# Kernel optimization log

Measured on AMD Instinct MI355X. Metric: run time of the kernel, lower is better.

Reference implementation:

```python
import jax, jax.numpy as jnp
import numpy as np

EMPHASIS_FACTOR = 1.5

def setup_inputs() -> dict:
    key = jax.random.key(0)
    k1, k2 = jax.random.split(key)
    B, T, F = 32, 4096, 256
    x = jax.random.normal(k1, (B, T, F), dtype=jnp.float32)
    W = jax.random.normal(k2, (F, 1), dtype=jnp.float32) * (1.0 / np.sqrt(F))
    b = jnp.zeros((1,), dtype=jnp.float32)
    return {"x": x, "W": W, "b": b}

def reference(x, W, b):
    # x: [B, T, F], W: [F, 1], b: [1]
    B, T, F = x.shape
    e = jnp.tanh(x @ W + b)                 # [B, T, 1]
    a = jax.nn.softmax(e, axis=1)           # softmax over time
    a_flat = a[..., 0]                      # [B, T]
    k = max(1, int(T * 0.1))
    _, top_idx = jax.lax.top_k(a_flat, k)   # [B, k]
    # scatter True at top-k positions (instead of O(T*k) broadcast compare)
    mask = jnp.zeros((B, T), dtype=bool).at[jnp.arange(B)[:, None], top_idx].set(True)
    a_emph = jnp.where(mask[..., None], a * EMPHASIS_FACTOR, a)  # [B, T, 1]
    return jnp.sum(x * a_emph, axis=1, keepdims=True)            # [B, 1, F]
```

## Files before the change

### kernel.cpp

```cpp
#include <hip/hip_runtime.h>
#include <math.h>

#define BB 32
#define TT 4096
#define FF 256
#define CH 64
#define NC (TT / CH)
#define K_TOP 409
#define EMPH_HALF 0.5f

__device__ __forceinline__ unsigned flip_key(float v) {
    unsigned u = __float_as_uint(v);
    return (u & 0x80000000u) ? ~u : (u | 0x80000000u);
}
__device__ __forceinline__ float unflip_key(unsigned k) {
    unsigned u = (k & 0x80000000u) ? (k & 0x7fffffffu) : ~k;
    return __uint_as_float(u);
}
__device__ __forceinline__ float fast_tanh(float z) {
    z = fminf(fmaxf(z, -15.f), 15.f);
    const float t = __expf(2.f * z);
    return (t - 1.f) * __builtin_amdgcn_rcpf(t + 1.f);
}

__global__ __launch_bounds__(256) void fused_pass1(const float* __restrict__ x,
                                                   const float* __restrict__ W,
                                                   const float* __restrict__ bias,
                                                   float* __restrict__ e,
                                                   float* __restrict__ P,
                                                   float* __restrict__ cm,
                                                   float* __restrict__ cs) {
    const int b = blockIdx.x / NC;
    const int c = blockIdx.x % NC;
    const int tid = threadIdx.x;
    const int wv = tid >> 6, ln = tid & 63;

    const float* xc = x + ((size_t)b * TT + (size_t)c * CH) * FF;
    const float4 wvec = ((const float4*)W)[ln];
    const float  bb   = bias[0];

    float4 acc = make_float4(0.f, 0.f, 0.f, 0.f);
    float  m = -1e30f, ssum = 0.f;

    #pragma unroll
    for (int s0 = 0; s0 < CH; s0 += 16) {
        const int r0 = s0 + wv * 4;
        float4 xr[4];
        #pragma unroll
        for (int i = 0; i < 4; i++)
            xr[i] = ((const float4*)(xc + (size_t)(r0 + i) * FF))[ln];

        float dv[4];
        #pragma unroll
        for (int i = 0; i < 4; i++)
            dv[i] = xr[i].x * wvec.x + xr[i].y * wvec.y +
                    xr[i].z * wvec.z + xr[i].w * wvec.w;
        #pragma unroll
        for (int i = 0; i < 4; i++) {
            float d = dv[i];
            #pragma unroll
            for (int off = 32; off; off >>= 1) d += __shfl_xor(d, off);
            dv[i] = fast_tanh(d + bb);
        }
        if (ln == 0)
            *(float4*)(e + (size_t)b * TT + c * CH + r0) =
                make_float4(dv[0], dv[1], dv[2], dv[3]);

        float lm = m;
        #pragma unroll
        for (int i = 0; i < 4; i++) lm = fmaxf(lm, dv[i]);
        const float alpha = __expf(m - lm);
        acc.x *= alpha; acc.y *= alpha; acc.z *= alpha; acc.w *= alpha;
        ssum *= alpha;
        #pragma unroll
        for (int i = 0; i < 4; i++) {
            const float wgt = __expf(dv[i] - lm);
            ssum += wgt;
            acc.x += wgt * xr[i].x; acc.y += wgt * xr[i].y;
            acc.z += wgt * xr[i].z; acc.w += wgt * xr[i].w;
        }
        m = lm;
    }

    __shared__ float4 part4[4][64];
    __shared__ float sm[4], ss4[4];
    part4[wv][ln] = acc;
    if (ln == 0) { sm[wv] = m; ss4[wv] = ssum; }
    __syncthreads();

    const float m0 = sm[0], m1 = sm[1], m2 = sm[2], m3 = sm[3];
    const float mc = fmaxf(fmaxf(m0, m1), fmaxf(m2, m3));
    const float s0s = __expf(m0 - mc), s1s = __expf(m1 - mc);
    const float s2s = __expf(m2 - mc), s3s = __expf(m3 - mc);
    const float* pf = (const float*)part4;
    const float p = pf[tid] * s0s + pf[256 + tid] * s1s +
                    pf[512 + tid] * s2s + pf[768 + tid] * s3s;
    P[((size_t)b * NC + c) * FF + tid] = p;
    if (tid == 0) {
        cm[b * NC + c] = mc;
        cs[b * NC + c] = ss4[0] * s0s + ss4[1] * s1s + ss4[2] * s2s + ss4[3] * s3s;
    }
}

__global__ __launch_bounds__(256) void select_combine(const float* __restrict__ x,
                                                      const float* __restrict__ e,
                                                      const float* __restrict__ P,
                                                      const float* __restrict__ cm,
                                                      const float* __restrict__ cs,
                                                      float* __restrict__ out) {
    const int b = blockIdx.x;
    const int tid = threadIdx.x;
    const int wv = tid >> 6, ln = tid & 63;

    __shared__ float sgm, sZ;
    __shared__ int   sc4[4];
    __shared__ float sscale[NC];
    __shared__ int   scount;
    __shared__ int   slist[TT];
    __shared__ float sval[TT];

    if (tid < 64) {
        const float mm = cm[b * NC + tid];
        const float ss = cs[b * NC + tid];
        float g = mm;
        #pragma unroll
        for (int off = 32; off; off >>= 1) g = fmaxf(g, __shfl_xor(g, off));
        float zz = ss * __expf(mm - g);
        #pragma unroll
        for (int off = 32; off; off >>= 1) zz += __shfl_xor(zz, off);
        if (tid == 0) { sgm = g; sZ = zz; scount = 0; }
    }

    const float* eb = e + (size_t)b * TT;
    unsigned key[16];
    #pragma unroll
    for (int j = 0; j < 16; j++) key[j] = flip_key(eb[tid + 256 * j]);
    __syncthreads();
    if (tid < 64) sscale[tid] = __expf(cm[b * NC + tid] - sgm);

    unsigned prefix = 0u, mask = 0u;
    int kk = K_TOP;
    for (int bit = 31; bit >= 0; bit--) {
        const unsigned bm = 1u << bit;
        const unsigned m2 = mask | bm;
        const unsigned want = prefix | bm;
        int cnt = 0;
        #pragma unroll
        for (int j = 0; j < 16; j++)
            cnt += (int)__popcll(__ballot((key[j] & m2) == want));
        __syncthreads();
        if (ln == 0) sc4[wv] = cnt;
        __syncthreads();
        const int tot = sc4[0] + sc4[1] + sc4[2] + sc4[3];
        if (tot >= kk) prefix = want; else kk -= tot;
        mask = m2;
    }
    const unsigned Kkey = prefix;

    float acc = 0.f;
    #pragma unroll 4
    for (int c = 0; c < NC; c++)
        acc += P[((size_t)b * NC + c) * FF + tid] * sscale[c];

    #pragma unroll
    for (int j = 0; j < 16; j++) {
        if (key[j] >= Kkey) {
            const int i = atomicAdd(&scount, 1);
            slist[i] = tid + 256 * j;
            sval[i]  = unflip_key(key[j]);
        }
    }
    __syncthreads();
    const int n = scount;
    for (int i = tid; i < n; i += 256)
        sval[i] = EMPH_HALF * __expf(sval[i] - sgm);
    __syncthreads();

    const float* xb = x + (size_t)b * TT * FF;
    for (int i = 0; i < n; i++)
        acc += sval[i] * xb[(size_t)slist[i] * FF + tid];

    out[b * FF + tid] = acc * (1.f / sZ);
}

extern "C" void kernel_launch(void* const* d_in, const int* in_sizes, int n_in,
                              void* d_out, int out_size, void* d_ws, size_t ws_size,
                              hipStream_t stream) {
    const float* x    = (const float*)d_in[0];
    const float* W    = (const float*)d_in[1];
    const float* bias = (const float*)d_in[2];
    float* out = (float*)d_out;

    float* e     = (float*)d_ws;
    float* P     = e + (size_t)BB * TT;
    float* cm    = P + (size_t)BB * NC * FF;
    float* cs    = cm + BB * NC;

    fused_pass1<<<BB * NC, 256, 0, stream>>>(x, W, bias, e, P, cm, cs);
    select_combine<<<BB, 256, 0, stream>>>(x, e, P, cm, cs, out);
}
```

Before: 231.0 us.

## Split select and combine into separate kernels, parallelize combine across time segments

The single per-batch select+combine kernel becomes two kernels. The first computes the radix-select threshold and softmax stats per batch and writes them to workspace. The second runs 16 blocks per batch, each handling a time segment, and accumulates into the output with atomics. The combine's strided gathers of selected rows were serialized over 32 blocks, and spreading them across more blocks raises parallelism. In exchange it adds a kernel launch, float atomics on the output, and summation order that can vary between runs.

```diff
diff --git a/kernel.cpp b/kernel.cpp
--- a/kernel.cpp
+++ b/kernel.cpp
@@ -8,6 +8,9 @@
 #define NC (TT / CH)
 #define K_TOP 409
 #define EMPH_HALF 0.5f
+#define NSEG 16
+#define SEGT (TT / NSEG)
+#define CPS (NC / NSEG)
 
 __device__ __forceinline__ unsigned flip_key(float v) {
     unsigned u = __float_as_uint(v);
@@ -102,22 +105,19 @@
     }
 }
 
-__global__ __launch_bounds__(256) void select_combine(const float* __restrict__ x,
-                                                      const float* __restrict__ e,
-                                                      const float* __restrict__ P,
-                                                      const float* __restrict__ cm,
-                                                      const float* __restrict__ cs,
-                                                      float* __restrict__ out) {
+__global__ __launch_bounds__(256) void select_kernel(const float* __restrict__ e,
+                                                     const float* __restrict__ cm,
+                                                     const float* __restrict__ cs,
+                                                     float* __restrict__ stats,
+                                                     float* __restrict__ out) {
     const int b = blockIdx.x;
     const int tid = threadIdx.x;
     const int wv = tid >> 6, ln = tid & 63;
 
+    out[b * FF + tid] = 0.f;
+
     __shared__ float sgm, sZ;
     __shared__ int   sc4[4];
-    __shared__ float sscale[NC];
-    __shared__ int   scount;
-    __shared__ int   slist[TT];
-    __shared__ float sval[TT];
 
     if (tid < 64) {
         const float mm = cm[b * NC + tid];
@@ -128,15 +128,13 @@
         float zz = ss * __expf(mm - g);
         #pragma unroll
         for (int off = 32; off; off >>= 1) zz += __shfl_xor(zz, off);
-        if (tid == 0) { sgm = g; sZ = zz; scount = 0; }
+        if (tid == 0) { sgm = g; sZ = zz; }
     }
 
     const float* eb = e + (size_t)b * TT;
     unsigned key[16];
     #pragma unroll
     for (int j = 0; j < 16; j++) key[j] = flip_key(eb[tid + 256 * j]);
-    __syncthreads();
-    if (tid < 64) sscale[tid] = __expf(cm[b * NC + tid] - sgm);
 
     unsigned prefix = 0u, mask = 0u;
     int kk = K_TOP;
@@ -155,32 +153,57 @@
         if (tot >= kk) prefix = want; else kk -= tot;
         mask = m2;
     }
-    const unsigned Kkey = prefix;
+
+    if (tid == 0) {
+        stats[3 * b + 0] = sgm;
+        stats[3 * b + 1] = sZ;
+        stats[3 * b + 2] = __uint_as_float(prefix);
+    }
+}
+
+__global__ __launch_bounds__(256) void combine_kernel(const float* __restrict__ x,
+                                                      const float* __restrict__ e,
+                                                      const float* __restrict__ P,
+                                                      const float* __restrict__ cm,
+                                                      const float* __restrict__ stats,
+                                                      float* __restrict__ out) {
+    const int b = blockIdx.x / NSEG;
+    const int s = blockIdx.x % NSEG;
+    const int tid = threadIdx.x;
+
+    const float gmax = stats[3 * b + 0];
+    const float Z    = stats[3 * b + 1];
+    const unsigned Kkey = __float_as_uint(stats[3 * b + 2]);
 
     float acc = 0.f;
-    #pragma unroll 4
-    for (int c = 0; c < NC; c++)
-        acc += P[((size_t)b * NC + c) * FF + tid] * sscale[c];
-
     #pragma unroll
-    for (int j = 0; j < 16; j++) {
-        if (key[j] >= Kkey) {
-            const int i = atomicAdd(&scount, 1);
-            slist[i] = tid + 256 * j;
-            sval[i]  = unflip_key(key[j]);
-        }
-    }
+    for (int c = 0; c < CPS; c++) {
+        const int cc = s * CPS + c;
+        const float sc2 = __expf(cm[b * NC + cc] - gmax);
+        acc += P[((size_t)b * NC + cc) * FF + tid] * sc2;
+    }
+
+    __shared__ int scount;
+    __shared__ int slist[SEGT];
+    __shared__ float sval[SEGT];
+    if (tid == 0) scount = 0;
     __syncthreads();
+
+    const int t = s * SEGT + tid;
+    const float ev = e[(size_t)b * TT + t];
+    if (flip_key(ev) >= Kkey) {
+        const int i = atomicAdd(&scount, 1);
+        slist[i] = t;
+        sval[i] = EMPH_HALF * __expf(ev - gmax);
+    }
+    __syncthreads();
+
     const int n = scount;
-    for (int i = tid; i < n; i += 256)
-        sval[i] = EMPH_HALF * __expf(sval[i] - sgm);
-    __syncthreads();
-
     const float* xb = x + (size_t)b * TT * FF;
     for (int i = 0; i < n; i++)
         acc += sval[i] * xb[(size_t)slist[i] * FF + tid];
 
-    out[b * FF + tid] = acc * (1.f / sZ);
+    atomicAdd(&out[b * FF + tid], acc * (1.f / Z));
 }
 
 extern "C" void kernel_launch(void* const* d_in, const int* in_sizes, int n_in,
@@ -195,7 +218,9 @@
     float* P     = e + (size_t)BB * TT;
     float* cm    = P + (size_t)BB * NC * FF;
     float* cs    = cm + BB * NC;
+    float* stats = cs + BB * NC;
 
     fused_pass1<<<BB * NC, 256, 0, stream>>>(x, W, bias, e, P, cm, cs);
-    select_combine<<<BB, 256, 0, stream>>>(x, e, P, cm, cs, out);
-}
+    select_kernel<<<BB, 256, 0, stream>>>(e, cm, cs, stats, out);
+    combine_kernel<<<BB * NSEG, 256, 0, stream>>>(x, e, P, cm, stats, out);
+}
```

Result: faster. 209.7 us (-9.2%).

## Split select/combine across time segments per batch with atomic output accumulation

Applied to the files above, without the earlier changes.

The second kernel now runs 16 blocks per batch instead of one. Each block redundantly computes the top-k threshold, then gathers only the selected rows in its own time segment and its share of the chunk partials, and adds its result into the output with atomicAdd. The output is zeroed in the first kernel. The radix-select loop drops one barrier per bit by giving each bit its own shared slot. The aim is to spread the serial gather over many more CUs, at the cost of repeating the threshold search and adding float atomics with nondeterministic summation order.

```diff
diff --git a/kernel.cpp b/kernel.cpp
--- a/kernel.cpp
+++ b/kernel.cpp
@@ -8,6 +8,9 @@
 #define NC (TT / CH)
 #define K_TOP 409
 #define EMPH_HALF 0.5f
+#define NSEG 16
+#define SEGT (TT / NSEG)
+#define CPS (NC / NSEG)
 
 __device__ __forceinline__ unsigned flip_key(float v) {
     unsigned u = __float_as_uint(v);
@@ -29,11 +32,14 @@
                                                    float* __restrict__ e,
                                                    float* __restrict__ P,
                                                    float* __restrict__ cm,
-                                                   float* __restrict__ cs) {
+                                                   float* __restrict__ cs,
+                                                   float* __restrict__ out) {
     const int b = blockIdx.x / NC;
     const int c = blockIdx.x % NC;
     const int tid = threadIdx.x;
     const int wv = tid >> 6, ln = tid & 63;
+
+    if (c == 0) out[b * FF + tid] = 0.f;
 
     const float* xc = x + ((size_t)b * TT + (size_t)c * CH) * FF;
     const float4 wvec = ((const float4*)W)[ln];
@@ -102,22 +108,24 @@
     }
 }
 
-__global__ __launch_bounds__(256) void select_combine(const float* __restrict__ x,
+__global__ __launch_bounds__(256) void combine_kernel(const float* __restrict__ x,
                                                       const float* __restrict__ e,
                                                       const float* __restrict__ P,
                                                       const float* __restrict__ cm,
                                                       const float* __restrict__ cs,
                                                       float* __restrict__ out) {
-    const int b = blockIdx.x;
+    const int b = blockIdx.x / NSEG;
+    const int s = blockIdx.x % NSEG;
     const int tid = threadIdx.x;
     const int wv = tid >> 6, ln = tid & 63;
 
     __shared__ float sgm, sZ;
-    __shared__ int   sc4[4];
-    __shared__ float sscale[NC];
+    __shared__ int   sc[32][4];
     __shared__ int   scount;
-    __shared__ int   slist[TT];
-    __shared__ float sval[TT];
+    __shared__ int   slist[SEGT];
+    __shared__ float sval[SEGT];
+
+    if (tid == 0) scount = 0;
 
     if (tid < 64) {
         const float mm = cm[b * NC + tid];
@@ -128,59 +136,58 @@
         float zz = ss * __expf(mm - g);
         #pragma unroll
         for (int off = 32; off; off >>= 1) zz += __shfl_xor(zz, off);
-        if (tid == 0) { sgm = g; sZ = zz; scount = 0; }
+        if (tid == 0) { sgm = g; sZ = zz; }
     }
 
     const float* eb = e + (size_t)b * TT;
     unsigned key[16];
     #pragma unroll
     for (int j = 0; j < 16; j++) key[j] = flip_key(eb[tid + 256 * j]);
+
     __syncthreads();
-    if (tid < 64) sscale[tid] = __expf(cm[b * NC + tid] - sgm);
+    const float gmax = sgm;
+    const float Zinv = 1.f / sZ;
+
+    float acc = 0.f;
+    #pragma unroll
+    for (int c = 0; c < CPS; c++) {
+        const int cc = s * CPS + c;
+        acc += P[((size_t)b * NC + cc) * FF + tid] * __expf(cm[b * NC + cc] - gmax);
+    }
 
     unsigned prefix = 0u, mask = 0u;
     int kk = K_TOP;
-    for (int bit = 31; bit >= 0; bit--) {
-        const unsigned bm = 1u << bit;
+    #pragma unroll 4
+    for (int it = 0; it < 32; it++) {
+        const unsigned bm = 1u << (31 - it);
         const unsigned m2 = mask | bm;
         const unsigned want = prefix | bm;
         int cnt = 0;
         #pragma unroll
         for (int j = 0; j < 16; j++)
             cnt += (int)__popcll(__ballot((key[j] & m2) == want));
+        if (ln == 0) sc[it][wv] = cnt;
         __syncthreads();
-        if (ln == 0) sc4[wv] = cnt;
-        __syncthreads();
-        const int tot = sc4[0] + sc4[1] + sc4[2] + sc4[3];
+        const int tot = sc[it][0] + sc[it][1] + sc[it][2] + sc[it][3];
         if (tot >= kk) prefix = want; else kk -= tot;
         mask = m2;
     }
     const unsigned Kkey = prefix;
 
-    float acc = 0.f;
-    #pragma unroll 4
-    for (int c = 0; c < NC; c++)
-        acc += P[((size_t)b * NC + c) * FF + tid] * sscale[c];
-
-    #pragma unroll
-    for (int j = 0; j < 16; j++) {
-        if (key[j] >= Kkey) {
-            const int i = atomicAdd(&scount, 1);
-            slist[i] = tid + 256 * j;
-            sval[i]  = unflip_key(key[j]);
-        }
+    const unsigned myk = key[s];
+    if (myk >= Kkey) {
+        const int i = atomicAdd(&scount, 1);
+        slist[i] = s * SEGT + tid;
+        sval[i]  = EMPH_HALF * __expf(unflip_key(myk) - gmax);
     }
     __syncthreads();
+
     const int n = scount;
-    for (int i = tid; i < n; i += 256)
-        sval[i] = EMPH_HALF * __expf(sval[i] - sgm);
-    __syncthreads();
-
     const float* xb = x + (size_t)b * TT * FF;
     for (int i = 0; i < n; i++)
         acc += sval[i] * xb[(size_t)slist[i] * FF + tid];
 
-    out[b * FF + tid] = acc * (1.f / sZ);
+    atomicAdd(&out[b * FF + tid], acc * Zinv);
 }
 
 extern "C" void kernel_launch(void* const* d_in, const int* in_sizes, int n_in,
@@ -191,11 +198,11 @@
     const float* bias = (const float*)d_in[2];
     float* out = (float*)d_out;
 
-    float* e     = (float*)d_ws;
-    float* P     = e + (size_t)BB * TT;
-    float* cm    = P + (size_t)BB * NC * FF;
-    float* cs    = cm + BB * NC;
-
-    fused_pass1<<<BB * NC, 256, 0, stream>>>(x, W, bias, e, P, cm, cs);
-    select_combine<<<BB, 256, 0, stream>>>(x, e, P, cm, cs, out);
-}
+    float* e  = (float*)d_ws;
+    float* P  = e + (size_t)BB * TT;
+    float* cm = P + (size_t)BB * NC * FF;
+    float* cs = cm + BB * NC;
+
+    fused_pass1<<<BB * NC, 256, 0, stream>>>(x, W, bias, e, P, cm, cs, out);
+    combine_kernel<<<BB * NSEG, 256, 0, stream>>>(x, e, P, cm, cs, out);
+}
```

New measurement: 210.5 us. 1.1x faster.
